# Optimization experiments

Measured on AMD Instinct MI355X. Metric: run time of the kernel, lower is better.

Reference implementation:

```python
import jax, jax.numpy as jnp
import numpy as np

EMB_DIM = 600
NN_UNITS = 300
K_FM = 5
B, L = 8, 2048


def fm(x, w0, w, V):
    # x: [B,L,F], w0: [1], w: [F], V: [k,F] -> [B,L,1]
    lin = w0 + x @ w[:, None]                      # [B,L,1]
    p1 = jnp.square(x @ V.T)                       # [B,L,k]
    p2 = jnp.square(x) @ jnp.square(V).T           # [B,L,k]
    inter = 0.5 * jnp.sum(p1 - p2, axis=-1, keepdims=True)
    return lin + inter


def setup_inputs() -> dict:
    key = jax.random.key(0)
    ks = jax.random.split(key, 12)
    s = 0.02
    inp = {
        "stack_input": jax.random.normal(ks[0], (2, B, L, EMB_DIM), jnp.float32),
        "W1": jax.random.normal(ks[1], (EMB_DIM, NN_UNITS), jnp.float32) * s,
        "b1": jnp.zeros((NN_UNITS,), jnp.float32),
        "W2": jax.random.normal(ks[2], (EMB_DIM, NN_UNITS), jnp.float32) * s,
        "b2": jnp.zeros((NN_UNITS,), jnp.float32),
        # FM params for the two concat branches (F = 2*EMB_DIM)
        "fm_cat_w0": jax.random.normal(ks[3], (2, 1), jnp.float32) * s,
        "fm_cat_w": jax.random.normal(ks[4], (2, 2 * EMB_DIM), jnp.float32) * s,
        "fm_cat_V": jax.random.normal(ks[5], (2, K_FM, 2 * EMB_DIM), jnp.float32) * s,
        # FM params for diff(passage,query) and mul(passage,query): order [p_diff, q_diff, p_mul, q_mul]
        "fm_dm_w0": jax.random.normal(ks[6], (4, 1), jnp.float32) * s,
        "fm_dm_w": jax.random.normal(ks[7], (4, EMB_DIM), jnp.float32) * s,
        "fm_dm_V": jax.random.normal(ks[8], (4, K_FM, EMB_DIM), jnp.float32) * s,
    }
    return inp


def reference(stack_input, W1, b1, W2, b2, fm_cat_w0, fm_cat_w, fm_cat_V,
              fm_dm_w0, fm_dm_w, fm_dm_V):
    passage = stack_input[0]   # [B,L,D]
    query = stack_input[1]     # [B,L,D]

    p_dense = jax.nn.relu(passage @ W1 + b1)   # [B,L,U]
    q_dense = jax.nn.relu(query @ W2 + b2)     # [B,L,U]

    scale = 1.0 / np.sqrt(EMB_DIM).astype(np.float32)
    affinity = scale * jnp.einsum('bpu,bqu->bpq', p_dense, q_dense)  # [B,Lp,Lq]

    aligned_p = jax.nn.softmax(affinity, axis=-1)                    # [B,Lp,Lq]
    aligned_q = jax.nn.softmax(jnp.swapaxes(affinity, 1, 2), axis=-1)  # [B,Lq,Lp]

    passage_aligned = jnp.einsum('bpq,bqd->bpd', aligned_p, passage)  # [B,Lp,D]
    query_aligned = jnp.einsum('bqp,bpd->bqd', aligned_q, query)      # [B,Lq,D]

    passage_concat = jnp.concatenate([query_aligned, passage], axis=2)
    query_concat = jnp.concatenate([passage_aligned, query], axis=2)
    passage_diff = query_aligned - passage
    query_diff = passage_aligned - query
    passage_mul = query_aligned * passage
    query_mul = passage_aligned * query

    c1 = fm(passage_concat, fm_cat_w0[0], fm_cat_w[0], fm_cat_V[0])
    c2 = fm(query_concat, fm_cat_w0[1], fm_cat_w[1], fm_cat_V[1])
    c3 = fm(passage_diff, fm_dm_w0[0], fm_dm_w[0], fm_dm_V[0])
    c4 = fm(query_diff, fm_dm_w0[1], fm_dm_w[1], fm_dm_V[1])
    c5 = fm(passage_mul, fm_dm_w0[2], fm_dm_w[2], fm_dm_V[2])
    c6 = fm(query_mul, fm_dm_w0[3], fm_dm_w[3], fm_dm_V[3])

    features_passage = jnp.concatenate([c1, c3, c5], axis=2)  # [B,L,3]
    features_query = jnp.concatenate([c2, c4, c6], axis=2)    # [B,L,3]
    return features_passage, features_query
```

## Files before the change

### kernel.cpp

```cpp
#include <hip/hip_runtime.h>
#include <hip/hip_bf16.h>

#define BATCH 8
#define LEN   2048
#define DIM   600
#define UNITS 300
#define BL    16384

typedef __attribute__((ext_vector_type(4))) float f32x4;
typedef __attribute__((ext_vector_type(8))) short s16x8;

#define PDB_OFF   0ULL
#define WT_OFF    20971520ULL
#define VT_OFF    21954560ULL
#define EXP_OFF   63897600ULL
#define EXPT_OFF  131006464ULL
#define PAB_OFF   198115328ULL
#define QAB_OFF   218038272ULL
#define RS_OFF    237961216ULL
#define CS_OFF    238026752ULL
#define WS_NEED   238092288ULL

#define AF_SCALE 0.040824829046386304f

__device__ __forceinline__ float wave_sum(float v) {
#pragma unroll
  for (int off = 32; off > 0; off >>= 1) v += __shfl_xor(v, off);
  return v;
}

__device__ __forceinline__ ushort f2bf(float f) {
  union { float f; uint u; } x; x.f = f;
  uint r = x.u + 0x7fffu + ((x.u >> 16) & 1u);
  return (ushort)(r >> 16);
}

__device__ __forceinline__ void ldbf8(const ushort* p, float* f) {
  uint4 q = *(const uint4*)p;
  f[0] = __uint_as_float(q.x << 16); f[1] = __uint_as_float(q.x & 0xffff0000u);
  f[2] = __uint_as_float(q.y << 16); f[3] = __uint_as_float(q.y & 0xffff0000u);
  f[4] = __uint_as_float(q.z << 16); f[5] = __uint_as_float(q.z & 0xffff0000u);
  f[6] = __uint_as_float(q.w << 16); f[7] = __uint_as_float(q.w & 0xffff0000u);
}
__device__ __forceinline__ void ldf8(const float* p, float* f) {
  float4 a = *(const float4*)p, b = *(const float4*)(p + 4);
  f[0]=a.x; f[1]=a.y; f[2]=a.z; f[3]=a.w; f[4]=b.x; f[5]=b.y; f[6]=b.z; f[7]=b.w;
}

__device__ __forceinline__ s16x8 pack8(float4 a, float4 b) {
  s16x8 r;
  r[0]=(short)f2bf(a.x); r[1]=(short)f2bf(a.y); r[2]=(short)f2bf(a.z); r[3]=(short)f2bf(a.w);
  r[4]=(short)f2bf(b.x); r[5]=(short)f2bf(b.y); r[6]=(short)f2bf(b.z); r[7]=(short)f2bf(b.w);
  return r;
}

__device__ __forceinline__ void gload_lds16(const void* g, void* l) {
  __builtin_amdgcn_global_load_lds(
      (const __attribute__((address_space(1))) unsigned int*)g,
      (__attribute__((address_space(3))) unsigned int*)l, 16, 0, 0);
}

__device__ __forceinline__ int eboff(int m, int n) {
  return m * 272 + ((((n >> 3) ^ ((m >> 3) & 7)) << 4) | ((n & 7) << 1));
}

__global__ __launch_bounds__(256) void prep_wt(const float* __restrict__ W1,
                                               const float* __restrict__ W2,
                                               char* __restrict__ wsb) {
  int id = blockIdx.x * 256 + threadIdx.x;
  if (id >= 2 * 384 * 80) return;
  int dir = id / (384 * 80); int rem = id % (384 * 80);
  int n = rem / 80, ko = rem % 80;
  const float* W = dir ? W2 : W1;
  s16x8 v;
#pragma unroll
  for (int e = 0; e < 8; e++) {
    int k = ko * 8 + e;
    float f = (n < 300 && k < 600) ? W[(size_t)k * 300 + n] : 0.f;
    v[e] = (short)f2bf(f);
  }
  ushort* wt = (ushort*)(wsb + WT_OFF) + (size_t)dir * 384 * 640 + (size_t)n * 640 + ko * 8;
  *(s16x8*)wt = v;
}

__global__ __launch_bounds__(256) void prep_vt(const float* __restrict__ stack,
                                               char* __restrict__ wsb) {
  int z = blockIdx.z;
  const float* src = stack + (size_t)z * LEN * DIM;
  ushort* dst = (ushort*)(wsb + VT_OFF) + (size_t)z * 640 * 2048;
  int p0 = blockIdx.x * 64, d0 = blockIdx.y * 64;
  __shared__ float tile[64][65];
  int t = threadIdx.x;
#pragma unroll
  for (int u = 0; u < 16; u++) {
    int id = u * 256 + t; int r = id >> 6, c = id & 63;
    tile[r][c] = (d0 + c < DIM) ? src[(size_t)(p0 + r) * DIM + d0 + c] : 0.f;
  }
  __syncthreads();
#pragma unroll
  for (int u = 0; u < 16; u++) {
    int id = u * 256 + t; int d = id >> 6, c = id & 63;
    dst[(size_t)(d0 + d) * 2048 + p0 + c] = f2bf(tile[c][d]);
  }
}

template<int MODE>
__global__ __launch_bounds__(256) void gemm_nt(const float* __restrict__ stack,
                                               const float* __restrict__ b1,
                                               const float* __restrict__ b2,
                                               char* __restrict__ wsb) {
  constexpr int KS = (MODE == 0) ? 10 : ((MODE == 1) ? 5 : 32);
  const int t = threadIdx.x;
  const int g = (t >> 4) & 3, l16 = t & 15;
  const int wv = t >> 6, wr = wv >> 1, wc = wv & 1;
  __shared__ __align__(16) char smem[34816];
  char* Ab = smem;
  char* Bb = smem + 16384;

  int bx, by, bz;
  {
    int bid = blockIdx.x;
    if constexpr (MODE == 0) {
      int s = (bid & 7) * 96 + (bid >> 3);
      bx = s % 3; by = (s / 3) & 127; bz = s / 384;
    } else if constexpr (MODE == 1) {
      int s = (bid & 7) * 256 + (bid >> 3);
      bx = s & 15; by = (s >> 4) & 15; bz = s >> 8;
    } else {
      int s = (bid & 7) * 160 + (bid >> 3);
      bx = s % 5; by = (s / 5) & 15; bz = s / 80;
    }
  }
  const int z = bz;
  const int m0 = by * 128, n0 = bx * 128;

  const float* Agf = nullptr;
  const ushort* Agb = nullptr;
  const ushort* Bgb = nullptr;
  int lda = 0, ldb = 0;
  int dir = 0, bat = 0;
  if constexpr (MODE == 0) {
    Agf = stack + (size_t)z * BL * DIM; lda = DIM;
    Bgb = (const ushort*)(wsb + WT_OFF) + (size_t)z * 384 * 640; ldb = 640;
  } else if constexpr (MODE == 1) {
    Agb = (const ushort*)(wsb + PDB_OFF) + (size_t)z * 2048 * 320; lda = 320;
    Bgb = (const ushort*)(wsb + PDB_OFF) + (size_t)16384 * 320 + (size_t)z * 2048 * 320; ldb = 320;
  } else {
    dir = z & 1; bat = z >> 1;
    Agb = (const ushort*)(wsb + (dir ? EXPT_OFF : EXP_OFF)) + (size_t)bat * 2048 * 2048; lda = 2048;
    Bgb = (const ushort*)(wsb + VT_OFF) + ((size_t)dir * 8 + bat) * 640 * 2048; ldb = 2048;
  }

  f32x4 acc[4][4];
#pragma unroll
  for (int i = 0; i < 4; i++)
#pragma unroll
    for (int j = 0; j < 4; j++) { f32x4 zz = {0.f, 0.f, 0.f, 0.f}; acc[i][j] = zz; }

  if constexpr (MODE == 0) {
    auto load_regs = [&](int k0, s16x8* va, s16x8* vb) {
#pragma unroll
      for (int u = 0; u < 4; u++) {
        int c = u * 256 + t; int row = c >> 3; int sl = c & 7; int gs = sl ^ (row & 7);
        int kb = k0 + gs * 8;
        if (kb < DIM) {
          const float* s = Agf + (size_t)(m0 + row) * DIM + kb;
          va[u] = pack8(*(const float4*)s, *(const float4*)(s + 4));
        } else {
          s16x8 zz = {0,0,0,0,0,0,0,0}; va[u] = zz;
        }
        vb[u] = *(const s16x8*)(Bgb + (size_t)(n0 + row) * ldb + k0 + gs * 8);
      }
    };
    s16x8 va[4], vb[4];
    load_regs(0, va, vb);
    for (int kt = 0; kt < KS; kt++) {
#pragma unroll
      for (int u = 0; u < 4; u++) {
        int c = u * 256 + t; int row = c >> 3; int sl = c & 7;
        *(s16x8*)(Ab + row * 128 + sl * 16) = va[u];
        *(s16x8*)(Bb + row * 128 + sl * 16) = vb[u];
      }
      __syncthreads();
      s16x8 na[4], nb[4];
      if (kt + 1 < KS) load_regs((kt + 1) * 64, na, nb);
#pragma unroll
      for (int ks = 0; ks < 2; ks++) {
        s16x8 af[4], bf[4];
#pragma unroll
        for (int f = 0; f < 4; f++) {
          int ar = wr * 64 + f * 16 + l16;
          af[f] = *(const s16x8*)(Ab + ar * 128 + (((ks * 4 + g) ^ (ar & 7)) * 16));
          int br = wc * 64 + f * 16 + l16;
          bf[f] = *(const s16x8*)(Bb + br * 128 + (((ks * 4 + g) ^ (br & 7)) * 16));
        }
#pragma unroll
        for (int i = 0; i < 4; i++)
#pragma unroll
          for (int j = 0; j < 4; j++)
            acc[i][j] = __builtin_amdgcn_mfma_f32_16x16x32_bf16(af[i], bf[j], acc[i][j], 0, 0, 0);
      }
      __syncthreads();
#pragma unroll
      for (int u = 0; u < 4; u++) { va[u] = na[u]; vb[u] = nb[u]; }
    }
  } else {
    for (int kt = 0; kt < KS; kt++) {
      int k0 = kt * 64;
#pragma unroll
      for (int u = 0; u < 4; u++) {
        int c = u * 256 + t; int row = c >> 3; int sl = c & 7; int gs = sl ^ (row & 7);
        char* dstA = Ab + (u * 256 + (t & 192)) * 16;
        char* dstB = Bb + (u * 256 + (t & 192)) * 16;
        gload_lds16(Agb + (size_t)(m0 + row) * lda + k0 + gs * 8, dstA);
        gload_lds16(Bgb + (size_t)(n0 + row) * ldb + k0 + gs * 8, dstB);
      }
      __syncthreads();
#pragma unroll
      for (int ks = 0; ks < 2; ks++) {
        s16x8 af[4], bf[4];
#pragma unroll
        for (int f = 0; f < 4; f++) {
          int ar = wr * 64 + f * 16 + l16;
          af[f] = *(const s16x8*)(Ab + ar * 128 + (((ks * 4 + g) ^ (ar & 7)) * 16));
          int br = wc * 64 + f * 16 + l16;
          bf[f] = *(const s16x8*)(Bb + br * 128 + (((ks * 4 + g) ^ (br & 7)) * 16));
        }
#pragma unroll
        for (int i = 0; i < 4; i++)
#pragma unroll
          for (int j = 0; j < 4; j++)
            acc[i][j] = __builtin_amdgcn_mfma_f32_16x16x32_bf16(af[i], bf[j], acc[i][j], 0, 0, 0);
      }
      __syncthreads();
    }
  }

  char* eb = smem;
  const float* bias = nullptr;
  const float* sums = nullptr;
  float* rowsum = nullptr; float* colsum = nullptr;
  if constexpr (MODE == 0) bias = z ? b2 : b1;
  if constexpr (MODE == 1) {
    rowsum = (float*)(wsb + RS_OFF) + (size_t)z * 2048;
    colsum = (float*)(wsb + CS_OFF) + (size_t)z * 2048;
  }
  if constexpr (MODE == 2)
    sums = (const float*)(wsb + (dir ? CS_OFF : RS_OFF)) + (size_t)bat * 2048;

  float colpart[4] = {0.f, 0.f, 0.f, 0.f};
#pragma unroll
  for (int fm = 0; fm < 4; fm++) {
#pragma unroll
    for (int i = 0; i < 4; i++) {
      int m = wr * 64 + fm * 16 + 4 * g + i;
      float inv = 1.f;
      if constexpr (MODE == 2) inv = 1.f / sums[m0 + m];
      float rowpart = 0.f;
#pragma unroll
      for (int fn = 0; fn < 4; fn++) {
        int n = wc * 64 + fn * 16 + l16;
        float v = acc[fm][fn][i];
        if constexpr (MODE == 0) {
          int gn = n0 + n;
          v = (gn < UNITS) ? fmaxf(v + bias[gn], 0.f) : 0.f;
        } else if constexpr (MODE == 1) {
          v = __expf(v * AF_SCALE);
          rowpart += v; colpart[fn] += v;
        } else {
          v *= inv;
        }
        *(ushort*)(eb + eboff(m, n)) = f2bf(v);
      }
      if constexpr (MODE == 1) {
        rowpart += __shfl_xor(rowpart, 1);
        rowpart += __shfl_xor(rowpart, 2);
        rowpart += __shfl_xor(rowpart, 4);
        rowpart += __shfl_xor(rowpart, 8);
        if (l16 == 0) atomicAdd(&rowsum[m0 + m], rowpart);
      }
    }
  }
  if constexpr (MODE == 1) {
#pragma unroll
    for (int fn = 0; fn < 4; fn++) {
      float cp = colpart[fn];
      cp += __shfl_xor(cp, 16);
      cp += __shfl_xor(cp, 32);
      if (((t >> 4) & 3) == 0)
        atomicAdd(&colsum[n0 + wc * 64 + fn * 16 + l16], cp);
    }
  }
  __syncthreads();

#pragma unroll
  for (int u = 0; u < 8; u++) {
    int id = u * 256 + t; int m = id >> 4; int cn = id & 15;
    s16x8 v = *(const s16x8*)(eb + m * 272 + ((cn ^ ((m >> 3) & 7)) << 4));
    int gn = n0 + cn * 8;
    if constexpr (MODE == 0) {
      if (gn < 320) {
        ushort* outp = (ushort*)(wsb + PDB_OFF) + (size_t)z * 16384 * 320;
        *(s16x8*)(outp + (size_t)(m0 + m) * 320 + gn) = v;
      }
    } else if constexpr (MODE == 1) {
      ushort* outp = (ushort*)(wsb + EXP_OFF) + (size_t)z * 2048 * 2048;
      *(s16x8*)(outp + (size_t)(m0 + m) * 2048 + gn) = v;
    } else {
      if (gn < 608) {
        ushort* outp = (ushort*)(wsb + (dir ? QAB_OFF : PAB_OFF)) + (size_t)bat * 2048 * 608;
        *(s16x8*)(outp + (size_t)(m0 + m) * 608 + gn) = v;
      }
    }
  }

  if constexpr (MODE == 1) {
    ushort* outpT = (ushort*)(wsb + EXPT_OFF) + (size_t)z * 2048 * 2048;
#pragma unroll
    for (int u = 0; u < 8; u++) {
      int id = u * 256 + t; int n = id >> 4; int mb = (id & 15) * 8;
      s16x8 v;
#pragma unroll
      for (int e = 0; e < 8; e++)
        v[e] = *(const short*)(eb + eboff(mb + e, n));
      *(s16x8*)(outpT + (size_t)(n0 + n) * 2048 + m0 + mb) = v;
    }
  }
}

__global__ __launch_bounds__(256) void fm_v2(
    const float* __restrict__ stack, const char* __restrict__ wsb,
    const float* __restrict__ cat_w0, const float* __restrict__ cat_w,
    const float* __restrict__ cat_V, const float* __restrict__ dm_w0,
    const float* __restrict__ dm_w, const float* __restrict__ dm_V,
    float* __restrict__ out)
{
  const int lane = threadIdx.x & 63;
  const int gw = blockIdx.x * 4 + (threadIdx.x >> 6);
  const int branch = gw >> 14;
  const int pos = gw & 16383;
  const ushort* x1 = (const ushort*)(wsb + (branch ? PAB_OFF : QAB_OFF)) + (size_t)pos * 608;
  const float* x2 = stack + (size_t)branch * BL * DIM + (size_t)pos * DIM;
  float* o = out + (size_t)branch * (BL * 3) + (size_t)pos * 3;

  {
    const float* w = cat_w + branch * 1200;
    const float* V = cat_V + (size_t)branch * 6000;
    float accW = 0.f, accP[5] = {}, accQ[5] = {};
    for (int oc = lane; oc < 150; oc += 64) {
      float x[8];
      if (oc < 75) ldbf8(x1 + oc * 8, x);
      else         ldf8(x2 + (oc - 75) * 8, x);
      float wv[8]; ldf8(w + oc * 8, wv);
#pragma unroll
      for (int e = 0; e < 8; e++) accW = fmaf(x[e], wv[e], accW);
#pragma unroll
      for (int k = 0; k < 5; k++) {
        float vv[8]; ldf8(V + k * 1200 + oc * 8, vv);
#pragma unroll
        for (int e = 0; e < 8; e++) {
          float xv = x[e] * vv[e];
          accP[k] += xv;
          accQ[k] = fmaf(xv, xv, accQ[k]);
        }
      }
    }
    float r = wave_sum(accW); float inter = 0.f;
#pragma unroll
    for (int k = 0; k < 5; k++) {
      float P = wave_sum(accP[k]), Q = wave_sum(accQ[k]);
      inter += P * P - Q;
    }
    if (lane == 0) o[0] = cat_w0[branch] + r + 0.5f * inter;
  }
#pragma unroll
  for (int which = 0; which < 2; which++) {
    const int idx = which * 2 + branch;
    const float* w = dm_w + idx * 600;
    const float* V = dm_V + (size_t)idx * 3000;
    float accW = 0.f, accP[5] = {}, accQ[5] = {};
    for (int oc = lane; oc < 75; oc += 64) {
      float a[8], b[8], x[8];
      ldbf8(x1 + oc * 8, a);
      ldf8(x2 + oc * 8, b);
#pragma unroll
      for (int e = 0; e < 8; e++) x[e] = which ? a[e] * b[e] : a[e] - b[e];
      float wv[8]; ldf8(w + oc * 8, wv);
#pragma unroll
      for (int e = 0; e < 8; e++) accW = fmaf(x[e], wv[e], accW);
#pragma unroll
      for (int k = 0; k < 5; k++) {
        float vv[8]; ldf8(V + k * 600 + oc * 8, vv);
#pragma unroll
        for (int e = 0; e < 8; e++) {
          float xv = x[e] * vv[e];
          accP[k] += xv;
          accQ[k] = fmaf(xv, xv, accQ[k]);
        }
      }
    }
    float r = wave_sum(accW); float inter = 0.f;
#pragma unroll
    for (int k = 0; k < 5; k++) {
      float P = wave_sum(accP[k]), Q = wave_sum(accQ[k]);
      inter += P * P - Q;
    }
    if (lane == 0) o[1 + which] = dm_w0[idx] + r + 0.5f * inter;
  }
}

#define PD_OFF   0UL
#define QD_OFF   4915200UL
#define PA_OFF   9830400UL
#define QA_OFF   19660800UL
#define A_OFF    29491200UL
#define ROWM_OFF 33685504UL
#define ROWS_OFF 33687552UL
#define COLM_OFF 33689600UL
#define COLS_OFF 33691648UL
#define PCM_OFF  33693696UL
#define PCS_OFF  33726464UL

__global__ __launch_bounds__(256) void dense_kernel(
    const float* __restrict__ stack, const float* __restrict__ W1,
    const float* __restrict__ b1, const float* __restrict__ W2,
    const float* __restrict__ b2, float* __restrict__ ws)
{
  const int dir = blockIdx.z;
  const float* X = stack + (size_t)dir * BL * DIM;
  const float* W = dir ? W2 : W1;
  const float* bias = dir ? b2 : b1;
  float* C = ws + (dir ? QD_OFF : PD_OFF);
  const int m0 = blockIdx.y * 64;
  const int n0 = blockIdx.x * 64;
  __shared__ float As[32][68];
  __shared__ float Bs[32][68];
  const int t = threadIdx.x;
  const int tx = t & 15, ty = t >> 4;
  float acc[4][4] = {};
  for (int k0 = 0; k0 < DIM; k0 += 32) {
#pragma unroll
    for (int i = 0; i < 8; i++) {
      int idx = i * 256 + t;
      int m = idx >> 5, k = idx & 31;
      int kk = k0 + k;
      As[k][m] = (kk < DIM) ? X[(size_t)(m0 + m) * DIM + kk] : 0.f;
    }
#pragma unroll
    for (int i = 0; i < 8; i++) {
      int idx = i * 256 + t;
      int k = idx >> 6, n = idx & 63;
      int kk = k0 + k, nn = n0 + n;
      Bs[k][n] = (kk < DIM && nn < UNITS) ? W[(size_t)kk * UNITS + nn] : 0.f;
    }
    __syncthreads();
#pragma unroll
    for (int k = 0; k < 32; k++) {
      float a[4], bb[4];
#pragma unroll
      for (int i = 0; i < 4; i++) a[i] = As[k][ty * 4 + i];
#pragma unroll
      for (int j = 0; j < 4; j++) bb[j] = Bs[k][tx * 4 + j];
#pragma unroll
      for (int i = 0; i < 4; i++)
#pragma unroll
        for (int j = 0; j < 4; j++)
          acc[i][j] = fmaf(a[i], bb[j], acc[i][j]);
    }
    __syncthreads();
  }
#pragma unroll
  for (int j = 0; j < 4; j++) {
    int nn = n0 + tx * 4 + j;
    if (nn >= UNITS) continue;
    float bv = bias[nn];
#pragma unroll
    for (int i = 0; i < 4; i++) {
      int mm = m0 + ty * 4 + i;
      float v = acc[i][j] + bv;
      C[(size_t)mm * UNITS + nn] = v > 0.f ? v : 0.f;
    }
  }
}

__global__ __launch_bounds__(256) void affinity_kernel(float* __restrict__ ws, int b)
{
  const float* P = ws + PD_OFF + (size_t)b * LEN * UNITS;
  const float* Q = ws + QD_OFF + (size_t)b * LEN * UNITS;
  float* A = ws + A_OFF;
  const int p0 = blockIdx.y * 64;
  const int q0 = blockIdx.x * 64;
  __shared__ float As[32][68], Bs[32][68];
  const int t = threadIdx.x, tx = t & 15, ty = t >> 4;
  float acc[4][4] = {};
  for (int k0 = 0; k0 < UNITS; k0 += 32) {
#pragma unroll
    for (int i = 0; i < 8; i++) {
      int idx = i * 256 + t;
      int m = idx >> 5, k = idx & 31;
      int kk = k0 + k;
      As[k][m] = (kk < UNITS) ? P[(size_t)(p0 + m) * UNITS + kk] : 0.f;
      Bs[k][m] = (kk < UNITS) ? Q[(size_t)(q0 + m) * UNITS + kk] : 0.f;
    }
    __syncthreads();
#pragma unroll
    for (int k = 0; k < 32; k++) {
      float a[4], bb[4];
#pragma unroll
      for (int i = 0; i < 4; i++) a[i] = As[k][ty * 4 + i];
#pragma unroll
      for (int j = 0; j < 4; j++) bb[j] = Bs[k][tx * 4 + j];
#pragma unroll
      for (int i = 0; i < 4; i++)
#pragma unroll
        for (int j = 0; j < 4; j++)
          acc[i][j] = fmaf(a[i], bb[j], acc[i][j]);
    }
    __syncthreads();
  }
#pragma unroll
  for (int i = 0; i < 4; i++)
#pragma unroll
    for (int j = 0; j < 4; j++)
      A[(size_t)(p0 + ty * 4 + i) * LEN + (q0 + tx * 4 + j)] = acc[i][j] * AF_SCALE;
}

__global__ __launch_bounds__(256) void rowstats_kernel(float* __restrict__ ws)
{
  const float* A = ws + A_OFF;
  float* rowM = ws + ROWM_OFF;
  float* rowS = ws + ROWS_OFF;
  const int p = blockIdx.x;
  const int t = threadIdx.x;
  __shared__ float row[2048];
  __shared__ float red[256];
#pragma unroll
  for (int i = 0; i < 8; i++) row[i * 256 + t] = A[(size_t)p * LEN + i * 256 + t];
  __syncthreads();
  float pm = -3.0e38f;
#pragma unroll
  for (int i = 0; i < 8; i++) pm = fmaxf(pm, row[i * 256 + t]);
  red[t] = pm; __syncthreads();
  for (int off = 128; off > 0; off >>= 1) {
    if (t < off) red[t] = fmaxf(red[t], red[t + off]);
    __syncthreads();
  }
  float m = red[0];
  __syncthreads();
  float ps = 0.f;
#pragma unroll
  for (int i = 0; i < 8; i++) ps += __expf(row[i * 256 + t] - m);
  red[t] = ps; __syncthreads();
  for (int off = 128; off > 0; off >>= 1) {
    if (t < off) red[t] += red[t + off];
    __syncthreads();
  }
  if (t == 0) { rowM[p] = m; rowS[p] = 1.f / red[0]; }
}

__global__ __launch_bounds__(256) void colpart_kernel(float* __restrict__ ws)
{
  const float* A = ws + A_OFF;
  float* pcm = ws + PCM_OFF;
  float* pcs = ws + PCS_OFF;
  const int q = blockIdx.x * 256 + threadIdx.x;
  const int chunk = blockIdx.y;
  const int p0 = chunk * 128;
  float m = -3.0e38f, s = 0.f;
  for (int p = p0; p < p0 + 128; p++) {
    float v = A[(size_t)p * LEN + q];
    float nm = fmaxf(m, v);
    s = s * __expf(m - nm) + __expf(v - nm);
    m = nm;
  }
  pcm[chunk * 2048 + q] = m;
  pcs[chunk * 2048 + q] = s;
}

__global__ __launch_bounds__(256) void colcomb_kernel(float* __restrict__ ws)
{
  const float* pcm = ws + PCM_OFF;
  const float* pcs = ws + PCS_OFF;
  float* colM = ws + COLM_OFF;
  float* colS = ws + COLS_OFF;
  const int q = blockIdx.x * 256 + threadIdx.x;
  float m = -3.0e38f;
#pragma unroll
  for (int c = 0; c < 16; c++) m = fmaxf(m, pcm[c * 2048 + q]);
  float s = 0.f;
#pragma unroll
  for (int c = 0; c < 16; c++) s += pcs[c * 2048 + q] * __expf(pcm[c * 2048 + q] - m);
  colM[q] = m;
  colS[q] = 1.f / s;
}

__global__ __launch_bounds__(256) void aligned_kernel(const float* __restrict__ stack,
                                                      float* __restrict__ ws, int b)
{
  const int transA = blockIdx.z;
  const float* A = ws + A_OFF;
  const float* stM = ws + (transA ? COLM_OFF : ROWM_OFF);
  const float* stS = ws + (transA ? COLS_OFF : ROWS_OFF);
  const float* V = stack + (size_t)transA * BL * DIM + (size_t)b * LEN * DIM;
  float* O = ws + (transA ? QA_OFF : PA_OFF) + (size_t)b * LEN * DIM;
  const int m0 = blockIdx.y * 64;
  const int n0 = blockIdx.x * 64;
  __shared__ float As[32][68], Bs[32][68];
  __shared__ float sM[64], sS[64];
  const int t = threadIdx.x, tx = t & 15, ty = t >> 4;
  if (t < 64) { sM[t] = stM[m0 + t]; sS[t] = stS[m0 + t]; }
  __syncthreads();
  float acc[4][4] = {};
  for (int k0 = 0; k0 < LEN; k0 += 32) {
    if (!transA) {
#pragma unroll
      for (int i = 0; i < 8; i++) {
        int idx = i * 256 + t;
        int m = idx >> 5, k = idx & 31;
        float a = A[(size_t)(m0 + m) * LEN + k0 + k];
        As[k][m] = __expf(a - sM[m]) * sS[m];
      }
    } else {
#pragma unroll
      for (int i = 0; i < 8; i++) {
        int idx = i * 256 + t;
        int k = idx >> 6, m = idx & 63;
        float a = A[(size_t)(k0 + k) * LEN + m0 + m];
        As[k][m] = __expf(a - sM[m]) * sS[m];
      }
    }
#pragma unroll
    for (int i = 0; i < 8; i++) {
      int idx = i * 256 + t;
      int k = idx >> 6, n = idx & 63;
      int nn = n0 + n;
      Bs[k][n] = (nn < DIM) ? V[(size_t)(k0 + k) * DIM + nn] : 0.f;
    }
    __syncthreads();
#pragma unroll
    for (int k = 0; k < 32; k++) {
      float a[4], bb[4];
#pragma unroll
      for (int i = 0; i < 4; i++) a[i] = As[k][ty * 4 + i];
#pragma unroll
      for (int j = 0; j < 4; j++) bb[j] = Bs[k][tx * 4 + j];
#pragma unroll
      for (int i = 0; i < 4; i++)
#pragma unroll
        for (int j = 0; j < 4; j++)
          acc[i][j] = fmaf(a[i], bb[j], acc[i][j]);
    }
    __syncthreads();
  }
#pragma unroll
  for (int i = 0; i < 4; i++)
#pragma unroll
    for (int j = 0; j < 4; j++) {
      int nn = n0 + tx * 4 + j;
      if (nn < DIM) O[(size_t)(m0 + ty * 4 + i) * DIM + nn] = acc[i][j];
    }
}

__global__ __launch_bounds__(256) void fm_kernel(
    const float* __restrict__ stack, const float* __restrict__ ws,
    const float* __restrict__ cat_w0, const float* __restrict__ cat_w,
    const float* __restrict__ cat_V, const float* __restrict__ dm_w0,
    const float* __restrict__ dm_w, const float* __restrict__ dm_V,
    float* __restrict__ out)
{
  const int lane = threadIdx.x & 63;
  const int gw = blockIdx.x * 4 + (threadIdx.x >> 6);
  const int branch = gw >> 14;
  const int pos = gw & 16383;
  const float* x1 = ws + (branch ? PA_OFF : QA_OFF) + (size_t)pos * DIM;
  const float* x2 = stack + (size_t)branch * BL * DIM + (size_t)pos * DIM;
  float* o = out + (size_t)branch * (BL * 3) + (size_t)pos * 3;
  {
    const float* w = cat_w + branch * 1200;
    const float* Vm = cat_V + branch * 6000;
    float accW = 0.f, accP[5] = {}, accQ[5] = {};
    for (int j = lane; j < 1200; j += 64) {
      float x = (j < 600) ? x1[j] : x2[j - 600];
      accW = fmaf(x, w[j], accW);
      float xx = x * x;
#pragma unroll
      for (int k = 0; k < 5; k++) {
        float v = Vm[k * 1200 + j];
        accP[k] = fmaf(x, v, accP[k]);
        accQ[k] = fmaf(xx, v * v, accQ[k]);
      }
    }
    accW = wave_sum(accW);
    float inter = 0.f;
#pragma unroll
    for (int k = 0; k < 5; k++) {
      float P = wave_sum(accP[k]);
      float Qv = wave_sum(accQ[k]);
      inter += P * P - Qv;
    }
    if (lane == 0) o[0] = cat_w0[branch] + accW + 0.5f * inter;
  }
  {
    const float* w = dm_w + branch * 600;
    const float* Vm = dm_V + branch * 3000;
    float accW = 0.f, accP[5] = {}, accQ[5] = {};
    for (int j = lane; j < 600; j += 64) {
      float x = x1[j] - x2[j];
      accW = fmaf(x, w[j], accW);
      float xx = x * x;
#pragma unroll
      for (int k = 0; k < 5; k++) {
        float v = Vm[k * 600 + j];
        accP[k] = fmaf(x, v, accP[k]);
        accQ[k] = fmaf(xx, v * v, accQ[k]);
      }
    }
    accW = wave_sum(accW);
    float inter = 0.f;
#pragma unroll
    for (int k = 0; k < 5; k++) {
      float P = wave_sum(accP[k]);
      float Qv = wave_sum(accQ[k]);
      inter += P * P - Qv;
    }
    if (lane == 0) o[1] = dm_w0[branch] + accW + 0.5f * inter;
  }
  {
    const int idx4 = 2 + branch;
    const float* w = dm_w + idx4 * 600;
    const float* Vm = dm_V + idx4 * 3000;
    float accW = 0.f, accP[5] = {}, accQ[5] = {};
    for (int j = lane; j < 600; j += 64) {
      float x = x1[j] * x2[j];
      accW = fmaf(x, w[j], accW);
      float xx = x * x;
#pragma unroll
      for (int k = 0; k < 5; k++) {
        float v = Vm[k * 600 + j];
        accP[k] = fmaf(x, v, accP[k]);
        accQ[k] = fmaf(xx, v * v, accQ[k]);
      }
    }
    accW = wave_sum(accW);
    float inter = 0.f;
#pragma unroll
    for (int k = 0; k < 5; k++) {
      float P = wave_sum(accP[k]);
      float Qv = wave_sum(accQ[k]);
      inter += P * P - Qv;
    }
    if (lane == 0) o[2] = dm_w0[idx4] + accW + 0.5f * inter;
  }
}

extern "C" void kernel_launch(void* const* d_in, const int* in_sizes, int n_in,
                              void* d_out, int out_size, void* d_ws, size_t ws_size,
                              hipStream_t stream) {
  const float* stack  = (const float*)d_in[0];
  const float* W1     = (const float*)d_in[1];
  const float* b1     = (const float*)d_in[2];
  const float* W2     = (const float*)d_in[3];
  const float* b2     = (const float*)d_in[4];
  const float* cat_w0 = (const float*)d_in[5];
  const float* cat_w  = (const float*)d_in[6];
  const float* cat_V  = (const float*)d_in[7];
  const float* dm_w0  = (const float*)d_in[8];
  const float* dm_w   = (const float*)d_in[9];
  const float* dm_V   = (const float*)d_in[10];
  float* out = (float*)d_out;

  if (ws_size >= WS_NEED) {
    char* wsb = (char*)d_ws;
    hipMemsetAsync(wsb + RS_OFF, 0, 131072, stream);
    prep_wt<<<240, 256, 0, stream>>>(W1, W2, wsb);
    prep_vt<<<dim3(32, 10, 16), 256, 0, stream>>>(stack, wsb);
    gemm_nt<0><<<768, 256, 0, stream>>>(stack, b1, b2, wsb);
    gemm_nt<1><<<2048, 256, 0, stream>>>(stack, b1, b2, wsb);
    gemm_nt<2><<<1280, 256, 0, stream>>>(stack, b1, b2, wsb);
    fm_v2<<<8192, 256, 0, stream>>>(stack, wsb, cat_w0, cat_w, cat_V,
                                    dm_w0, dm_w, dm_V, out);
  } else {
    float* ws = (float*)d_ws;
    dense_kernel<<<dim3(5, 256, 2), 256, 0, stream>>>(stack, W1, b1, W2, b2, ws);
    for (int b = 0; b < BATCH; b++) {
      affinity_kernel<<<dim3(32, 32), 256, 0, stream>>>(ws, b);
      rowstats_kernel<<<2048, 256, 0, stream>>>(ws);
      colpart_kernel<<<dim3(8, 16), 256, 0, stream>>>(ws);
      colcomb_kernel<<<8, 256, 0, stream>>>(ws);
      aligned_kernel<<<dim3(10, 32, 2), 256, 0, stream>>>(stack, ws, b);
    }
    fm_kernel<<<8192, 256, 0, stream>>>(stack, ws, cat_w0, cat_w, cat_V,
                                        dm_w0, dm_w, dm_V, out);
  }
}
```

Baseline: 563.3 us.

## Double-buffer LDS in MFMA GEMMs, merge prep kernels, widen transpose reads

The MODE 1/2 GEMMs now double-buffer their shared-memory tiles. The next K tile is issued with global_load_lds while the current one is computed, and partial vmcnt waits plus raw s_barrier replace __syncthreads. The two prep kernels are merged into one launch. The transposed exp write now reads 32-bit pairs and emits two rows per iteration. These changes aim to hide global latency and cut launch and LDS read overhead, at the cost of doubling LDS to 64KB per block in MODE 1/2, which may lower occupancy.

```diff
diff --git a/kernel.cpp b/kernel.cpp
--- a/kernel.cpp
+++ b/kernel.cpp
@@ -64,43 +64,44 @@
   return m * 272 + ((((n >> 3) ^ ((m >> 3) & 7)) << 4) | ((n & 7) << 1));
 }
 
-__global__ __launch_bounds__(256) void prep_wt(const float* __restrict__ W1,
-                                               const float* __restrict__ W2,
-                                               char* __restrict__ wsb) {
-  int id = blockIdx.x * 256 + threadIdx.x;
-  if (id >= 2 * 384 * 80) return;
-  int dir = id / (384 * 80); int rem = id % (384 * 80);
-  int n = rem / 80, ko = rem % 80;
-  const float* W = dir ? W2 : W1;
-  s16x8 v;
-#pragma unroll
-  for (int e = 0; e < 8; e++) {
-    int k = ko * 8 + e;
-    float f = (n < 300 && k < 600) ? W[(size_t)k * 300 + n] : 0.f;
-    v[e] = (short)f2bf(f);
-  }
-  ushort* wt = (ushort*)(wsb + WT_OFF) + (size_t)dir * 384 * 640 + (size_t)n * 640 + ko * 8;
-  *(s16x8*)wt = v;
-}
-
-__global__ __launch_bounds__(256) void prep_vt(const float* __restrict__ stack,
-                                               char* __restrict__ wsb) {
-  int z = blockIdx.z;
-  const float* src = stack + (size_t)z * LEN * DIM;
-  ushort* dst = (ushort*)(wsb + VT_OFF) + (size_t)z * 640 * 2048;
-  int p0 = blockIdx.x * 64, d0 = blockIdx.y * 64;
-  __shared__ float tile[64][65];
+__global__ __launch_bounds__(256) void prep_all(const float* __restrict__ stack,
+                                                const float* __restrict__ W1,
+                                                const float* __restrict__ W2,
+                                                char* __restrict__ wsb) {
+  int b = blockIdx.x;
   int t = threadIdx.x;
-#pragma unroll
-  for (int u = 0; u < 16; u++) {
-    int id = u * 256 + t; int r = id >> 6, c = id & 63;
-    tile[r][c] = (d0 + c < DIM) ? src[(size_t)(p0 + r) * DIM + d0 + c] : 0.f;
-  }
-  __syncthreads();
-#pragma unroll
-  for (int u = 0; u < 16; u++) {
-    int id = u * 256 + t; int d = id >> 6, c = id & 63;
-    dst[(size_t)(d0 + d) * 2048 + p0 + c] = f2bf(tile[c][d]);
+  if (b < 5120) {
+    int z = b / 320; int r = b % 320;
+    int p0 = (r & 31) * 64, d0 = (r >> 5) * 64;
+    const float* src = stack + (size_t)z * LEN * DIM;
+    ushort* dst = (ushort*)(wsb + VT_OFF) + (size_t)z * 640 * 2048;
+    __shared__ float tile[64][65];
+#pragma unroll
+    for (int u = 0; u < 16; u++) {
+      int id = u * 256 + t; int rr = id >> 6, c = id & 63;
+      tile[rr][c] = (d0 + c < DIM) ? src[(size_t)(p0 + rr) * DIM + d0 + c] : 0.f;
+    }
+    __syncthreads();
+#pragma unroll
+    for (int u = 0; u < 16; u++) {
+      int id = u * 256 + t; int d = id >> 6, c = id & 63;
+      dst[(size_t)(d0 + d) * 2048 + p0 + c] = f2bf(tile[c][d]);
+    }
+  } else {
+    int id = (b - 5120) * 256 + t;
+    if (id >= 2 * 384 * 80) return;
+    int dir = id / (384 * 80); int rem = id % (384 * 80);
+    int n = rem / 80, ko = rem % 80;
+    const float* W = dir ? W2 : W1;
+    s16x8 v;
+#pragma unroll
+    for (int e = 0; e < 8; e++) {
+      int k = ko * 8 + e;
+      float f = (n < 300 && k < 600) ? W[(size_t)k * 300 + n] : 0.f;
+      v[e] = (short)f2bf(f);
+    }
+    ushort* wt = (ushort*)(wsb + WT_OFF) + (size_t)dir * 384 * 640 + (size_t)n * 640 + ko * 8;
+    *(s16x8*)wt = v;
   }
 }
 
@@ -113,9 +114,7 @@
   const int t = threadIdx.x;
   const int g = (t >> 4) & 3, l16 = t & 15;
   const int wv = t >> 6, wr = wv >> 1, wc = wv & 1;
-  __shared__ __align__(16) char smem[34816];
-  char* Ab = smem;
-  char* Bb = smem + 16384;
+  __shared__ __align__(16) char smem[(MODE == 0) ? 34816 : 65536];
 
   int bx, by, bz;
   {
@@ -158,6 +157,8 @@
     for (int j = 0; j < 4; j++) { f32x4 zz = {0.f, 0.f, 0.f, 0.f}; acc[i][j] = zz; }
 
   if constexpr (MODE == 0) {
+    char* Ab = smem;
+    char* Bb = smem + 16384;
     auto load_regs = [&](int k0, s16x8* va, s16x8* vb) {
 #pragma unroll
       for (int u = 0; u < 4; u++) {
@@ -181,7 +182,8 @@
         *(s16x8*)(Ab + row * 128 + sl * 16) = va[u];
         *(s16x8*)(Bb + row * 128 + sl * 16) = vb[u];
       }
-      __syncthreads();
+      asm volatile("s_waitcnt lgkmcnt(0)" ::: "memory");
+      __builtin_amdgcn_s_barrier();
       s16x8 na[4], nb[4];
       if (kt + 1 < KS) load_regs((kt + 1) * 64, na, nb);
 #pragma unroll
@@ -200,31 +202,46 @@
           for (int j = 0; j < 4; j++)
             acc[i][j] = __builtin_amdgcn_mfma_f32_16x16x32_bf16(af[i], bf[j], acc[i][j], 0, 0, 0);
       }
-      __syncthreads();
+      asm volatile("" ::: "memory");
+      __builtin_amdgcn_s_barrier();
 #pragma unroll
       for (int u = 0; u < 4; u++) { va[u] = na[u]; vb[u] = nb[u]; }
     }
   } else {
+    auto STAGE = [&](int buf, int kt) {
+      int k0 = kt * 64;
+      char* Ad = smem + buf * 32768;
+      char* Bd = Ad + 16384;
+#pragma unroll
+      for (int u = 0; u < 4; u++) {
+        int c = u * 256 + t; int row = c >> 3; int gs = (c & 7) ^ (row & 7);
+        gload_lds16(Agb + (size_t)(m0 + row) * lda + k0 + gs * 8,
+                    Ad + (u * 256 + (t & 192)) * 16);
+        gload_lds16(Bgb + (size_t)(n0 + row) * ldb + k0 + gs * 8,
+                    Bd + (u * 256 + (t & 192)) * 16);
+      }
+    };
+    STAGE(0, 0);
+    int cur = 0;
     for (int kt = 0; kt < KS; kt++) {
-      int k0 = kt * 64;
-#pragma unroll
-      for (int u = 0; u < 4; u++) {
-        int c = u * 256 + t; int row = c >> 3; int sl = c & 7; int gs = sl ^ (row & 7);
-        char* dstA = Ab + (u * 256 + (t & 192)) * 16;
-        char* dstB = Bb + (u * 256 + (t & 192)) * 16;
-        gload_lds16(Agb + (size_t)(m0 + row) * lda + k0 + gs * 8, dstA);
-        gload_lds16(Bgb + (size_t)(n0 + row) * ldb + k0 + gs * 8, dstB);
-      }
-      __syncthreads();
+      if (kt + 1 < KS) {
+        STAGE(cur ^ 1, kt + 1);
+        asm volatile("s_waitcnt vmcnt(8)" ::: "memory");
+      } else {
+        asm volatile("s_waitcnt vmcnt(0)" ::: "memory");
+      }
+      __builtin_amdgcn_s_barrier();
+      char* Ar = smem + cur * 32768;
+      char* Br = Ar + 16384;
 #pragma unroll
       for (int ks = 0; ks < 2; ks++) {
         s16x8 af[4], bf[4];
 #pragma unroll
         for (int f = 0; f < 4; f++) {
           int ar = wr * 64 + f * 16 + l16;
-          af[f] = *(const s16x8*)(Ab + ar * 128 + (((ks * 4 + g) ^ (ar & 7)) * 16));
+          af[f] = *(const s16x8*)(Ar + ar * 128 + (((ks * 4 + g) ^ (ar & 7)) * 16));
           int br = wc * 64 + f * 16 + l16;
-          bf[f] = *(const s16x8*)(Bb + br * 128 + (((ks * 4 + g) ^ (br & 7)) * 16));
+          bf[f] = *(const s16x8*)(Br + br * 128 + (((ks * 4 + g) ^ (br & 7)) * 16));
         }
 #pragma unroll
         for (int i = 0; i < 4; i++)
@@ -232,7 +249,9 @@
           for (int j = 0; j < 4; j++)
             acc[i][j] = __builtin_amdgcn_mfma_f32_16x16x32_bf16(af[i], bf[j], acc[i][j], 0, 0, 0);
       }
-      __syncthreads();
+      asm volatile("" ::: "memory");
+      __builtin_amdgcn_s_barrier();
+      cur ^= 1;
     }
   }
 
@@ -317,13 +336,22 @@
   if constexpr (MODE == 1) {
     ushort* outpT = (ushort*)(wsb + EXPT_OFF) + (size_t)z * 2048 * 2048;
 #pragma unroll
-    for (int u = 0; u < 8; u++) {
-      int id = u * 256 + t; int n = id >> 4; int mb = (id & 15) * 8;
-      s16x8 v;
+    for (int u = 0; u < 4; u++) {
+      int id = u * 256 + t; int n2 = id >> 4; int mb = (id & 15) * 8;
+      int n = n2 * 2;
+      uint w[8];
 #pragma unroll
       for (int e = 0; e < 8; e++)
-        v[e] = *(const short*)(eb + eboff(mb + e, n));
-      *(s16x8*)(outpT + (size_t)(n0 + n) * 2048 + m0 + mb) = v;
+        w[e] = *(const uint*)(eb + eboff(mb + e, n));
+      union { uint u4[4]; s16x8 v; } lo, hi;
+#pragma unroll
+      for (int p = 0; p < 4; p++) {
+        uint a = w[2 * p], b = w[2 * p + 1];
+        lo.u4[p] = (a & 0xffffu) | (b << 16);
+        hi.u4[p] = (a >> 16) | (b & 0xffff0000u);
+      }
+      *(s16x8*)(outpT + (size_t)(n0 + n) * 2048 + m0 + mb) = lo.v;
+      *(s16x8*)(outpT + (size_t)(n0 + n + 1) * 2048 + m0 + mb) = hi.v;
     }
   }
 }
@@ -772,8 +800,7 @@
   if (ws_size >= WS_NEED) {
     char* wsb = (char*)d_ws;
     hipMemsetAsync(wsb + RS_OFF, 0, 131072, stream);
-    prep_wt<<<240, 256, 0, stream>>>(W1, W2, wsb);
-    prep_vt<<<dim3(32, 10, 16), 256, 0, stream>>>(stack, wsb);
+    prep_all<<<5360, 256, 0, stream>>>(stack, W1, W2, wsb);
     gemm_nt<0><<<768, 256, 0, stream>>>(stack, b1, b2, wsb);
     gemm_nt<1><<<2048, 256, 0, stream>>>(stack, b1, b2, wsb);
     gemm_nt<2><<<1280, 256, 0, stream>>>(stack, b1, b2, wsb);
```

Measured after the change: 528.0 us. 6.3% less time.
